# Kernel tuning notes

Hardware: AMD Instinct MI355X
Metric: run time of the kernel (lower is better)

## Reference

```python
import jax, jax.numpy as jnp
import numpy as np

N_NODES = 100000
N_EDGES = 1600000
DIM = 128
N_BUNDLES = 8
BUNDLE_DIM = 4
HIDDEN = 256
TIME = 2


def setup_inputs() -> dict:
    key = jax.random.key(0)
    ks = jax.random.split(key, 8)
    x = jax.random.normal(ks[0], (N_NODES, DIM), dtype=jnp.float32)
    node_rep = jax.random.normal(ks[1], (N_NODES, N_BUNDLES, BUNDLE_DIM, BUNDLE_DIM), dtype=jnp.float32)
    # edge list; ensure every node has out-degree >= 1 so degree norm is finite
    src_extra = jax.random.randint(ks[2], (N_EDGES - N_NODES,), 0, N_NODES)
    src = jnp.concatenate([jnp.arange(N_NODES), src_extra]).astype(jnp.int64)
    dst = jax.random.randint(ks[3], (N_EDGES,), 0, N_NODES).astype(jnp.int64)
    w1 = jax.random.normal(ks[4], (HIDDEN, DIM), dtype=jnp.float32) * (1.0 / np.sqrt(DIM))
    b1 = jnp.zeros((HIDDEN,), dtype=jnp.float32)
    w2 = jax.random.normal(ks[5], (DIM, HIDDEN), dtype=jnp.float32) * (1.0 / np.sqrt(HIDDEN))
    b2 = jnp.zeros((DIM,), dtype=jnp.float32)
    return {"x": x, "node_rep": node_rep, "src": src, "dst": dst,
            "w1": w1, "b1": b1, "w2": w2, "b2": b2}


def reference(x, node_rep, src, dst, w1, b1, w2, b2):
    n = x.shape[0]
    # out-degrees (number of edges with node as source)
    deg = jax.ops.segment_sum(jnp.ones_like(src, dtype=x.dtype), src, num_segments=n)
    # u_mul_v: per-edge product of src and dst degrees -> symmetric norm coefs
    norm_coefs = jax.lax.rsqrt(deg[src] * deg[dst])  # [E]
    # per-bundle rotation: einsum('abcd,abde->abce', node_rep, vf)
    vf = x.reshape(n, N_BUNDLES, BUNDLE_DIM, -1)
    vf = jnp.einsum('nbcd,nbde->nbce', node_rep, vf)
    h = vf.reshape(n, DIM)
    # u_mul_e_sum repeated `time` times: out[dst] += h[src] * coef
    for _ in range(TIME):
        h = jax.ops.segment_sum(h[src] * norm_coefs[:, None], dst, num_segments=n)
    # inverse rotation with transposed node_rep
    vf = h.reshape(n, N_BUNDLES, BUNDLE_DIM, -1)
    vf = jnp.einsum('nbdc,nbde->nbce', node_rep, vf)
    h = vf.reshape(n, DIM)
    # feed-forward (dropout=0, exact GELU as in torch nn.GELU default)
    h = jax.nn.gelu(h @ w1.T + b1, approximate=False)
    return h @ w2.T + b2
```

## Files before the change

kernel.cpp:

```cpp
#include <hip/hip_runtime.h>
#include <hip/hip_bf16.h>
#include <math.h>

#define DIM 128
#define HID 256

typedef short s8x __attribute__((ext_vector_type(8)));
typedef float f4x __attribute__((ext_vector_type(4)));

__device__ __forceinline__ unsigned short f2bf(float f) {
    unsigned int u = __float_as_uint(f);
    u += 0x7FFF + ((u >> 16) & 1);
    return (unsigned short)(u >> 16);
}
__device__ __forceinline__ float bf2f(unsigned short b) {
    return __uint_as_float(((unsigned int)b) << 16);
}
__device__ __forceinline__ float bflo(unsigned int p) {
    return __uint_as_float(p << 16);
}
__device__ __forceinline__ float bfhi(unsigned int p) {
    return __uint_as_float(p & 0xffff0000u);
}


__global__ __launch_bounds__(256) void hist_rot_kernel(
        const int* __restrict__ src, const int* __restrict__ dst,
        int* __restrict__ TD, int* __restrict__ TS, int nE, int nbuck, int chunk,
        int NBE,
        const float* __restrict__ x, const float* __restrict__ R,
        unsigned short* __restrict__ h0,
        const float* __restrict__ w1, const float* __restrict__ w2,
        unsigned short* __restrict__ w1b, unsigned short* __restrict__ w2b,
        int n, int nbRot) {
    __shared__ int hd[1024], hs[1024];
    const int tid = threadIdx.x, blk = blockIdx.x;

    if (blk >= NBE) {
        const int rb = blk - NBE;
        if (rb >= nbRot) {
            int t = (rb - nbRot) * 256 + tid;
            for (int i = t; i < 32768; i += 4096) {
                w1b[i] = f2bf(w1[i]);
                w2b[i] = f2bf(w2[i]);
            }
            return;
        }
        int u = rb * 256 + tid;
        if (u >= n * 8) return;
        int nd = u >> 3, b = u & 7;
        const float* xp = &x[(size_t)nd * DIM + b * 16];
        const float* Rp = &R[(size_t)nd * DIM + b * 16];
        float xv[16], rv[16];
#pragma unroll
        for (int d = 0; d < 4; ++d) {
            *(float4*)&xv[d * 4] = *(const float4*)&xp[d * 4];
            *(float4*)&rv[d * 4] = *(const float4*)&Rp[d * 4];
        }
        unsigned short ob[16];
#pragma unroll
        for (int c = 0; c < 4; ++c)
#pragma unroll
            for (int e = 0; e < 4; ++e) {
                float acc = 0.f;
#pragma unroll
                for (int d = 0; d < 4; ++d) acc += rv[c * 4 + d] * xv[d * 4 + e];
                ob[c * 4 + e] = f2bf(acc);
            }
        unsigned short* op = &h0[(size_t)nd * DIM + b * 16];
        *(s8x*)&op[0] = *(s8x*)&ob[0];
        *(s8x*)&op[8] = *(s8x*)&ob[8];
        return;
    }

    for (int b = tid; b < nbuck; b += 256) { hd[b] = 0; hs[b] = 0; }
    __syncthreads();
    int beg = blk * chunk, end = min(beg + chunk, nE);
    for (int i = beg + tid; i < end; i += 256) {
        atomicAdd(&hd[dst[i] >> 7], 1);
        atomicAdd(&hs[src[i] >> 7], 1);
    }
    __syncthreads();
    for (int b = tid; b < nbuck; b += 256) {
        TD[b * NBE + blk] = hd[b];
        TS[b * NBE + blk] = hs[b];
    }
}

__global__ void scan_blocks(const int* in, int* out, int* bsums, int n) {
    __shared__ int part[256];
    const int tid = threadIdx.x;
    const int base = blockIdx.x * 1024 + tid * 4;
    int v[4];
    int sum = 0;
#pragma unroll
    for (int k = 0; k < 4; ++k) {
        v[k] = (base + k < n) ? in[base + k] : 0;
        sum += v[k];
    }
    part[tid] = sum;
    __syncthreads();
    for (int off = 1; off < 256; off <<= 1) {
        int t = (tid >= off) ? part[tid - off] : 0;
        __syncthreads();
        part[tid] += t;
        __syncthreads();
    }
    int excl = part[tid] - sum;
    if (tid == 255) bsums[blockIdx.x] = part[255];
#pragma unroll
    for (int k = 0; k < 4; ++k) {
        if (base + k < n) out[base + k] = excl;
        excl += v[k];
    }
}

__global__ void scan_sums(int* bsums, int nb) {
    __shared__ int part[256];
    const int tid = threadIdx.x;
    const int base = tid * 8;
    int v[8];
    int sum = 0;
#pragma unroll
    for (int k = 0; k < 8; ++k) {
        v[k] = (base + k < nb) ? bsums[base + k] : 0;
        sum += v[k];
    }
    part[tid] = sum;
    __syncthreads();
    for (int off = 1; off < 256; off <<= 1) {
        int t = (tid >= off) ? part[tid - off] : 0;
        __syncthreads();
        part[tid] += t;
        __syncthreads();
    }
    int excl = part[tid] - sum;
#pragma unroll
    for (int k = 0; k < 8; ++k) {
        if (base + k < nb) bsums[base + k] = excl;
        excl += v[k];
    }
}

__global__ void scan_add(int* T, const int* __restrict__ bsums, int n2, int half, int E) {
    int i = blockIdx.x * blockDim.x + threadIdx.x;
    if (i < n2) {
        int v = T[i] + bsums[i >> 10];
        T[i] = (i >= half) ? v - E : v;
    }
}

__global__ __launch_bounds__(256) void scatter_edges(
        const int* __restrict__ src, const int* __restrict__ dst,
        const int* __restrict__ TD, const int* __restrict__ TS,
        unsigned int* __restrict__ pairs, unsigned char* __restrict__ sbyte,
        int nE, int nbuck, int chunk, int NBE) {
    __shared__ int cd[1024], cs[1024];
    const int tid = threadIdx.x, blk = blockIdx.x;
    for (int b = tid; b < nbuck; b += 256) {
        cd[b] = TD[b * NBE + blk];
        cs[b] = TS[b * NBE + blk];
    }
    __syncthreads();
    int beg = blk * chunk, end = min(beg + chunk, nE);
    for (int i = beg + tid; i < end; i += 256) {
        int s = src[i], d = dst[i];
        int pd = atomicAdd(&cd[d >> 7], 1);
        pairs[pd] = ((unsigned)s << 7) | (unsigned)(d & 127);
        int ps = atomicAdd(&cs[s >> 7], 1);
        sbyte[ps] = (unsigned char)(s & 127);
    }
}

__global__ __launch_bounds__(256) void finalize_src(
        const unsigned char* __restrict__ sbyte, const int* __restrict__ TS,
        float* __restrict__ rdeg, int nE, int nbuck, int nN, int NBE) {
    __shared__ int hist[128];
    const int tid = threadIdx.x, b = blockIdx.x;
    if (tid < 128) hist[tid] = 0;
    __syncthreads();
    int beg = TS[b * NBE];
    int end = (b + 1 < nbuck) ? TS[(b + 1) * NBE] : nE;
    for (int i = beg + tid; i < end; i += 256)
        atomicAdd(&hist[sbyte[i]], 1);
    __syncthreads();
    if (tid < 128) {
        int idx = (b << 7) + tid;
        if (idx < nN) rdeg[idx] = rsqrtf((float)hist[tid]);
    }
}

template<bool PACK>
__global__ __launch_bounds__(256) void finalize_dst(
        const unsigned int* __restrict__ pairs, const int* __restrict__ TD,
        const float* __restrict__ rdeg,
        int* __restrict__ rowstart, uint2* __restrict__ ecsr,
        int* __restrict__ esrcA, int nE, int nbuck, int nN, int NBE) {
    __shared__ int hist[128], sbuf[128], cur[128];
    const int tid = threadIdx.x, b = blockIdx.x;
    int beg = TD[b * NBE];
    int end = (b + 1 < nbuck) ? TD[(b + 1) * NBE] : nE;
    if (tid < 128) hist[tid] = 0;
    __syncthreads();
    for (int i = beg + tid; i < end; i += 256)
        atomicAdd(&hist[(int)(pairs[i] & 127u)], 1);
    __syncthreads();
    int v = (tid < 128) ? hist[tid] : 0;
    if (tid < 128) sbuf[tid] = v;
    __syncthreads();
    for (int off = 1; off < 128; off <<= 1) {
        int t = (tid < 128 && tid >= off) ? sbuf[tid - off] : 0;
        __syncthreads();
        if (tid < 128) sbuf[tid] += t;
        __syncthreads();
    }
    if (tid < 128) {
        int excl = sbuf[tid] - v;
        cur[tid] = excl;
        int idx = (b << 7) + tid;
        if (idx <= nN) rowstart[idx] = beg + excl;
    }
    __syncthreads();
    for (int i = beg + tid; i < end; i += 256) {
        unsigned int p = pairs[i];
        int l = (int)(p & 127u);
        int s = (int)(p >> 7);
        int pos = atomicAdd(&cur[l], 1);
        if (PACK) {
            float coef = rdeg[s] * rdeg[(b << 7) + l];
            ecsr[beg + pos] = make_uint2((unsigned)s, __float_as_uint(coef));
        } else {
            esrcA[beg + pos] = s;
        }
    }
}

template<bool PACK, bool ROT>
__global__ __launch_bounds__(256) void gather_kernel(
        const unsigned short* __restrict__ hsrc,
        const uint2* __restrict__ ecsr, const int* __restrict__ esrcA,
        const float* __restrict__ rdeg, const int* __restrict__ rowstart,
        const float* __restrict__ R,
        unsigned short* __restrict__ hdst, int n) {
    const int node = blockIdx.x * 16 + (threadIdx.x >> 4);
    const int lane = threadIdx.x & 15;
    if (node >= n) return;
    const int beg = rowstart[node];
    const int end = rowstart[node + 1];
    float rd = 0.f;
    if (!PACK) rd = rdeg[node];

    float4 r0, r1;
    if (ROT) {
        r0 = *(const float4*)&R[(size_t)node * DIM + lane * 8];
        r1 = *(const float4*)&R[(size_t)node * DIM + lane * 8 + 4];
    }

    float a0 = 0.f, a1 = 0.f, a2 = 0.f, a3 = 0.f;
    float a4 = 0.f, a5 = 0.f, a6 = 0.f, a7 = 0.f;
    int i = beg;
    for (; i + 4 <= end; i += 4) {
        int s0, s1, s2, s3;
        float c0, c1, c2, c3;
        if (PACK) {
            uint2 e0 = ecsr[i], e1 = ecsr[i + 1], e2 = ecsr[i + 2], e3 = ecsr[i + 3];
            s0 = (int)e0.x; c0 = __uint_as_float(e0.y);
            s1 = (int)e1.x; c1 = __uint_as_float(e1.y);
            s2 = (int)e2.x; c2 = __uint_as_float(e2.y);
            s3 = (int)e3.x; c3 = __uint_as_float(e3.y);
        } else {
            s0 = esrcA[i]; s1 = esrcA[i + 1]; s2 = esrcA[i + 2]; s3 = esrcA[i + 3];
            c0 = rdeg[s0] * rd; c1 = rdeg[s1] * rd;
            c2 = rdeg[s2] * rd; c3 = rdeg[s3] * rd;
        }
        uint4 p0 = *(const uint4*)&hsrc[(size_t)s0 * DIM + lane * 8];
        uint4 p1 = *(const uint4*)&hsrc[(size_t)s1 * DIM + lane * 8];
        uint4 p2 = *(const uint4*)&hsrc[(size_t)s2 * DIM + lane * 8];
        uint4 p3 = *(const uint4*)&hsrc[(size_t)s3 * DIM + lane * 8];
        a0 += bflo(p0.x) * c0 + bflo(p1.x) * c1 + bflo(p2.x) * c2 + bflo(p3.x) * c3;
        a1 += bfhi(p0.x) * c0 + bfhi(p1.x) * c1 + bfhi(p2.x) * c2 + bfhi(p3.x) * c3;
        a2 += bflo(p0.y) * c0 + bflo(p1.y) * c1 + bflo(p2.y) * c2 + bflo(p3.y) * c3;
        a3 += bfhi(p0.y) * c0 + bfhi(p1.y) * c1 + bfhi(p2.y) * c2 + bfhi(p3.y) * c3;
        a4 += bflo(p0.z) * c0 + bflo(p1.z) * c1 + bflo(p2.z) * c2 + bflo(p3.z) * c3;
        a5 += bfhi(p0.z) * c0 + bfhi(p1.z) * c1 + bfhi(p2.z) * c2 + bfhi(p3.z) * c3;
        a6 += bflo(p0.w) * c0 + bflo(p1.w) * c1 + bflo(p2.w) * c2 + bflo(p3.w) * c3;
        a7 += bfhi(p0.w) * c0 + bfhi(p1.w) * c1 + bfhi(p2.w) * c2 + bfhi(p3.w) * c3;
    }
    for (; i < end; ++i) {
        int s0;
        float c0;
        if (PACK) {
            uint2 e0 = ecsr[i];
            s0 = (int)e0.x; c0 = __uint_as_float(e0.y);
        } else {
            s0 = esrcA[i];
            c0 = rdeg[s0] * rd;
        }
        uint4 p0 = *(const uint4*)&hsrc[(size_t)s0 * DIM + lane * 8];
        a0 += bflo(p0.x) * c0;
        a1 += bfhi(p0.x) * c0;
        a2 += bflo(p0.y) * c0;
        a3 += bfhi(p0.y) * c0;
        a4 += bflo(p0.z) * c0;
        a5 += bfhi(p0.z) * c0;
        a6 += bflo(p0.w) * c0;
        a7 += bfhi(p0.w) * c0;
    }

    unsigned short ob[8];
    if (ROT) {
        const int half = lane & 1;
        float av[8] = {a0, a1, a2, a3, a4, a5, a6, a7};
        float rown[8] = {r0.x, r0.y, r0.z, r0.w, r1.x, r1.y, r1.z, r1.w};
        float hb[16], rv[16];
#pragma unroll
        for (int j = 0; j < 8; ++j) {
            float ho = __shfl_xor(av[j], 1);
            float ro = __shfl_xor(rown[j], 1);
            hb[j]     = half ? ho      : av[j];
            hb[8 + j] = half ? av[j]   : ho;
            rv[j]     = half ? ro      : rown[j];
            rv[8 + j] = half ? rown[j] : ro;
        }
        float rr[2][4];
#pragma unroll
        for (int cc = 0; cc < 2; ++cc)
#pragma unroll
            for (int d = 0; d < 4; ++d)
                rr[cc][d] = half ? rv[d * 4 + 2 + cc] : rv[d * 4 + cc];
#pragma unroll
        for (int cc = 0; cc < 2; ++cc)
#pragma unroll
            for (int e = 0; e < 4; ++e) {
                float acc = 0.f;
#pragma unroll
                for (int d = 0; d < 4; ++d) acc += rr[cc][d] * hb[d * 4 + e];
                ob[cc * 4 + e] = f2bf(acc);
            }
    } else {
        ob[0] = f2bf(a0); ob[1] = f2bf(a1); ob[2] = f2bf(a2); ob[3] = f2bf(a3);
        ob[4] = f2bf(a4); ob[5] = f2bf(a5); ob[6] = f2bf(a6); ob[7] = f2bf(a7);
    }
    uint4 o;
    o.x = (unsigned)ob[0] | ((unsigned)ob[1] << 16);
    o.y = (unsigned)ob[2] | ((unsigned)ob[3] << 16);
    o.z = (unsigned)ob[4] | ((unsigned)ob[5] << 16);
    o.w = (unsigned)ob[6] | ((unsigned)ob[7] << 16);
    *(uint4*)&hdst[(size_t)node * DIM + lane * 8] = o;
}

#define ABST 136
#define HBST 264
__global__ __launch_bounds__(256, 4) void ffn_kernel(
        const unsigned short* __restrict__ h,
        const unsigned short* __restrict__ w1b,
        const float* __restrict__ b1,
        const unsigned short* __restrict__ w2b,
        const float* __restrict__ b2,
        float* __restrict__ out, int n) {
    __shared__ unsigned short smem[64 * HBST];
    unsigned short* abuf = smem;
    unsigned short* hbuf = smem;
    const int tid  = threadIdx.x;
    const int node0 = blockIdx.x * 64;
    const int wave = tid >> 6;
    const int lane = tid & 63;
    const int lr = lane & 15;
    const int lq = lane >> 4;

    for (int u = tid; u < 512; u += 256) {
        int nd = u >> 3, b = u & 7;
        int gn = node0 + nd;
        s8x v0 = {0,0,0,0,0,0,0,0}, v1 = {0,0,0,0,0,0,0,0};
        if (gn < n) {
            const unsigned short* hp = &h[(size_t)gn * DIM + b * 16];
            v0 = *(const s8x*)&hp[0];
            v1 = *(const s8x*)&hp[8];
        }
        *(s8x*)&abuf[nd * ABST + b * 16] = v0;
        *(s8x*)&abuf[nd * ABST + b * 16 + 8] = v1;
    }
    __syncthreads();

    f4x acc1[4][4];
#pragma unroll
    for (int mt = 0; mt < 4; ++mt)
#pragma unroll
        for (int nt = 0; nt < 4; ++nt) acc1[mt][nt] = (f4x){0.f, 0.f, 0.f, 0.f};

    const int nw = wave * 64;
    for (int ks = 0; ks < 4; ++ks) {
        const int k0 = ks * 32 + lq * 8;
        s8x af[4], bfv[4];
#pragma unroll
        for (int mt = 0; mt < 4; ++mt)
            af[mt] = *(const s8x*)&abuf[(mt * 16 + lr) * ABST + k0];
#pragma unroll
        for (int nt = 0; nt < 4; ++nt)
            bfv[nt] = *(const s8x*)&w1b[(size_t)(nw + nt * 16 + lr) * 128 + k0];
#pragma unroll
        for (int mt = 0; mt < 4; ++mt)
#pragma unroll
            for (int nt = 0; nt < 4; ++nt)
                acc1[mt][nt] = __builtin_amdgcn_mfma_f32_16x16x32_bf16(
                    af[mt], bfv[nt], acc1[mt][nt], 0, 0, 0);
    }
    __syncthreads();

#pragma unroll
    for (int nt = 0; nt < 4; ++nt) {
        int nn = nw + nt * 16 + lr;
        float bias = b1[nn];
#pragma unroll
        for (int mt = 0; mt < 4; ++mt) {
#pragma unroll
            for (int r = 0; r < 4; ++r) {
                float v = acc1[mt][nt][r] + bias;
                v = 0.5f * v * (1.f + erff(v * 0.70710678118654752f));
                hbuf[(mt * 16 + lq * 4 + r) * HBST + nn] = f2bf(v);
            }
        }
    }
    __syncthreads();

    f4x acc2[4][2];
#pragma unroll
    for (int mt = 0; mt < 4; ++mt)
#pragma unroll
        for (int nt = 0; nt < 2; ++nt) acc2[mt][nt] = (f4x){0.f, 0.f, 0.f, 0.f};

    const int nw2 = wave * 32;
    for (int ks = 0; ks < 8; ++ks) {
        const int k0 = ks * 32 + lq * 8;
        s8x af[4], bf2v[2];
#pragma unroll
        for (int mt = 0; mt < 4; ++mt)
            af[mt] = *(const s8x*)&hbuf[(mt * 16 + lr) * HBST + k0];
#pragma unroll
        for (int nt = 0; nt < 2; ++nt)
            bf2v[nt] = *(const s8x*)&w2b[(size_t)(nw2 + nt * 16 + lr) * 256 + k0];
#pragma unroll
        for (int mt = 0; mt < 4; ++mt)
#pragma unroll
            for (int nt = 0; nt < 2; ++nt)
                acc2[mt][nt] = __builtin_amdgcn_mfma_f32_16x16x32_bf16(
                    af[mt], bf2v[nt], acc2[mt][nt], 0, 0, 0);
    }
#pragma unroll
    for (int nt = 0; nt < 2; ++nt) {
        int n2 = nw2 + nt * 16 + lr;
        float bias = b2[n2];
#pragma unroll
        for (int mt = 0; mt < 4; ++mt) {
#pragma unroll
            for (int r = 0; r < 4; ++r) {
                int gn = node0 + mt * 16 + lq * 4 + r;
                if (gn < n) out[(size_t)gn * DIM + n2] = acc2[mt][nt][r] + bias;
            }
        }
    }
}

extern "C" void kernel_launch(void* const* d_in, const int* in_sizes, int n_in,
                              void* d_out, int out_size, void* d_ws, size_t ws_size,
                              hipStream_t stream) {
    const float* x   = (const float*)d_in[0];
    const float* R   = (const float*)d_in[1];
    const int*   src = (const int*)d_in[2];
    const int*   dst = (const int*)d_in[3];
    const float* w1  = (const float*)d_in[4];
    const float* b1  = (const float*)d_in[5];
    const float* w2  = (const float*)d_in[6];
    const float* b2  = (const float*)d_in[7];
    float* out = (float*)d_out;

    const int N = in_sizes[0] / DIM;
    const int E = in_sizes[2];

    const int nbuck = (N + 127) >> 7;
    const int NBE = 256;
    const int chunk = (E + NBE - 1) / NBE;
    const int nScan = nbuck * NBE;
    const int nScan2 = 2 * nScan;
    const int nbScan2 = (nScan2 + 1023) / 1024;

    unsigned short* hA = (unsigned short*)d_ws;
    unsigned short* hM = hA + (size_t)N * DIM;
    unsigned int*  pairs = (unsigned int*)hM;
    unsigned char* sbyte = (unsigned char*)(pairs + E);
    char* edge_base = (char*)(hM + (size_t)N * DIM);

    const size_t tail_bytes = (size_t)N * 4 + (size_t)(N + 1) * 4 +
                              (size_t)nScan * 8 + 2048 * 4 + (size_t)2 * 32768 * 2;
    const size_t fixed_bytes = (size_t)N * DIM * 4;
    const bool use_pack = (fixed_bytes + (size_t)E * 8 + tail_bytes) <= ws_size;
    const size_t edge_bytes = use_pack ? (size_t)E * 8 : (size_t)E * 4;

    uint2* ecsr  = (uint2*)edge_base;
    int*   esrcA = (int*)edge_base;
    char* q = edge_base + edge_bytes;
    float* rdeg     = (float*)q;
    int*   rowstart = (int*)(rdeg + N);
    int*   TD       = rowstart + (N + 1);
    int*   TS       = TD + nScan;
    int*   bsums    = TS + nScan;
    unsigned short* w1b = (unsigned short*)(bsums + 2048);
    unsigned short* w2b = w1b + 32768;

    const int BLK = 256;

    const int nbRot = ((size_t)N * 8 + BLK - 1) / BLK;
    hist_rot_kernel<<<NBE + nbRot + 16, BLK, 0, stream>>>(
        src, dst, TD, TS, E, nbuck, chunk, NBE,
        x, R, hA, w1, w2, w1b, w2b, N, nbRot);

    scan_blocks<<<nbScan2, BLK, 0, stream>>>(TD, TD, bsums, nScan2);
    scan_sums<<<1, BLK, 0, stream>>>(bsums, nbScan2);
    scan_add<<<(nScan2 + BLK - 1) / BLK, BLK, 0, stream>>>(TD, bsums, nScan2, nScan, E);
    scatter_edges<<<NBE, BLK, 0, stream>>>(src, dst, TD, TS, pairs, sbyte, E, nbuck, chunk, NBE);
    finalize_src<<<nbuck, BLK, 0, stream>>>(sbyte, TS, rdeg, E, nbuck, N, NBE);
    if (use_pack)
        finalize_dst<true><<<nbuck, BLK, 0, stream>>>(pairs, TD, rdeg, rowstart,
                                                      ecsr, esrcA, E, nbuck, N, NBE);
    else
        finalize_dst<false><<<nbuck, BLK, 0, stream>>>(pairs, TD, rdeg, rowstart,
                                                       ecsr, esrcA, E, nbuck, N, NBE);

    const int nbG = (N + 15) / 16;
    if (use_pack) {
        gather_kernel<true , false><<<nbG, BLK, 0, stream>>>(hA, ecsr, esrcA, rdeg,
                                                             rowstart, R, hM, N);
        gather_kernel<true , true ><<<nbG, BLK, 0, stream>>>(hM, ecsr, esrcA, rdeg,
                                                             rowstart, R, hA, N);
    } else {
        gather_kernel<false, false><<<nbG, BLK, 0, stream>>>(hA, ecsr, esrcA, rdeg,
                                                             rowstart, R, hM, N);
        gather_kernel<false, true ><<<nbG, BLK, 0, stream>>>(hM, ecsr, esrcA, rdeg,
                                                             rowstart, R, hA, N);
    }

    ffn_kernel<<<(N + 63) / 64, BLK, 0, stream>>>(hA, w1b, b1, w2b, b2, out, N);
}
```

Baseline: 418.7 us.

## Unroll edge histogram/scatter and SpMM gather; load FFN A-tiles directly from global

```diff
diff --git a/kernel.cpp b/kernel.cpp
--- a/kernel.cpp
+++ b/kernel.cpp
@@ -76,7 +76,16 @@
     for (int b = tid; b < nbuck; b += 256) { hd[b] = 0; hs[b] = 0; }
     __syncthreads();
     int beg = blk * chunk, end = min(beg + chunk, nE);
-    for (int i = beg + tid; i < end; i += 256) {
+    int i = beg + tid;
+    for (; i + 256 < end; i += 512) {
+        int d0 = dst[i], d1 = dst[i + 256];
+        int s0 = src[i], s1 = src[i + 256];
+        atomicAdd(&hd[d0 >> 7], 1);
+        atomicAdd(&hd[d1 >> 7], 1);
+        atomicAdd(&hs[s0 >> 7], 1);
+        atomicAdd(&hs[s1 >> 7], 1);
+    }
+    if (i < end) {
         atomicAdd(&hd[dst[i] >> 7], 1);
         atomicAdd(&hs[src[i] >> 7], 1);
     }
@@ -163,7 +172,20 @@
     }
     __syncthreads();
     int beg = blk * chunk, end = min(beg + chunk, nE);
-    for (int i = beg + tid; i < end; i += 256) {
+    int i = beg + tid;
+    for (; i + 256 < end; i += 512) {
+        int s0 = src[i], d0 = dst[i];
+        int s1 = src[i + 256], d1 = dst[i + 256];
+        int pd0 = atomicAdd(&cd[d0 >> 7], 1);
+        pairs[pd0] = ((unsigned)s0 << 7) | (unsigned)(d0 & 127);
+        int pd1 = atomicAdd(&cd[d1 >> 7], 1);
+        pairs[pd1] = ((unsigned)s1 << 7) | (unsigned)(d1 & 127);
+        int ps0 = atomicAdd(&cs[s0 >> 7], 1);
+        sbyte[ps0] = (unsigned char)(s0 & 127);
+        int ps1 = atomicAdd(&cs[s1 >> 7], 1);
+        sbyte[ps1] = (unsigned char)(s1 & 127);
+    }
+    if (i < end) {
         int s = src[i], d = dst[i];
         int pd = atomicAdd(&cd[d >> 7], 1);
         pairs[pd] = ((unsigned)s << 7) | (unsigned)(d & 127);
@@ -259,6 +281,53 @@
     float a0 = 0.f, a1 = 0.f, a2 = 0.f, a3 = 0.f;
     float a4 = 0.f, a5 = 0.f, a6 = 0.f, a7 = 0.f;
     int i = beg;
+    for (; i + 8 <= end; i += 8) {
+        int s0, s1, s2, s3, s4, s5, s6, s7;
+        float c0, c1, c2, c3, c4, c5, c6, c7;
+        if (PACK) {
+            uint2 e0 = ecsr[i],     e1 = ecsr[i + 1], e2 = ecsr[i + 2], e3 = ecsr[i + 3];
+            uint2 e4 = ecsr[i + 4], e5 = ecsr[i + 5], e6 = ecsr[i + 6], e7 = ecsr[i + 7];
+            s0 = (int)e0.x; c0 = __uint_as_float(e0.y);
+            s1 = (int)e1.x; c1 = __uint_as_float(e1.y);
+            s2 = (int)e2.x; c2 = __uint_as_float(e2.y);
+            s3 = (int)e3.x; c3 = __uint_as_float(e3.y);
+            s4 = (int)e4.x; c4 = __uint_as_float(e4.y);
+            s5 = (int)e5.x; c5 = __uint_as_float(e5.y);
+            s6 = (int)e6.x; c6 = __uint_as_float(e6.y);
+            s7 = (int)e7.x; c7 = __uint_as_float(e7.y);
+        } else {
+            s0 = esrcA[i];     s1 = esrcA[i + 1]; s2 = esrcA[i + 2]; s3 = esrcA[i + 3];
+            s4 = esrcA[i + 4]; s5 = esrcA[i + 5]; s6 = esrcA[i + 6]; s7 = esrcA[i + 7];
+            c0 = rdeg[s0] * rd; c1 = rdeg[s1] * rd;
+            c2 = rdeg[s2] * rd; c3 = rdeg[s3] * rd;
+            c4 = rdeg[s4] * rd; c5 = rdeg[s5] * rd;
+            c6 = rdeg[s6] * rd; c7 = rdeg[s7] * rd;
+        }
+        uint4 p0 = *(const uint4*)&hsrc[(size_t)s0 * DIM + lane * 8];
+        uint4 p1 = *(const uint4*)&hsrc[(size_t)s1 * DIM + lane * 8];
+        uint4 p2 = *(const uint4*)&hsrc[(size_t)s2 * DIM + lane * 8];
+        uint4 p3 = *(const uint4*)&hsrc[(size_t)s3 * DIM + lane * 8];
+        uint4 p4 = *(const uint4*)&hsrc[(size_t)s4 * DIM + lane * 8];
+        uint4 p5 = *(const uint4*)&hsrc[(size_t)s5 * DIM + lane * 8];
+        uint4 p6 = *(const uint4*)&hsrc[(size_t)s6 * DIM + lane * 8];
+        uint4 p7 = *(const uint4*)&hsrc[(size_t)s7 * DIM + lane * 8];
+        a0 += bflo(p0.x) * c0 + bflo(p1.x) * c1 + bflo(p2.x) * c2 + bflo(p3.x) * c3
+            + bflo(p4.x) * c4 + bflo(p5.x) * c5 + bflo(p6.x) * c6 + bflo(p7.x) * c7;
+        a1 += bfhi(p0.x) * c0 + bfhi(p1.x) * c1 + bfhi(p2.x) * c2 + bfhi(p3.x) * c3
+            + bfhi(p4.x) * c4 + bfhi(p5.x) * c5 + bfhi(p6.x) * c6 + bfhi(p7.x) * c7;
+        a2 += bflo(p0.y) * c0 + bflo(p1.y) * c1 + bflo(p2.y) * c2 + bflo(p3.y) * c3
+            + bflo(p4.y) * c4 + bflo(p5.y) * c5 + bflo(p6.y) * c6 + bflo(p7.y) * c7;
+        a3 += bfhi(p0.y) * c0 + bfhi(p1.y) * c1 + bfhi(p2.y) * c2 + bfhi(p3.y) * c3
+            + bfhi(p4.y) * c4 + bfhi(p5.y) * c5 + bfhi(p6.y) * c6 + bfhi(p7.y) * c7;
+        a4 += bflo(p0.z) * c0 + bflo(p1.z) * c1 + bflo(p2.z) * c2 + bflo(p3.z) * c3
+            + bflo(p4.z) * c4 + bflo(p5.z) * c5 + bflo(p6.z) * c6 + bflo(p7.z) * c7;
+        a5 += bfhi(p0.z) * c0 + bfhi(p1.z) * c1 + bfhi(p2.z) * c2 + bfhi(p3.z) * c3
+            + bfhi(p4.z) * c4 + bfhi(p5.z) * c5 + bfhi(p6.z) * c6 + bfhi(p7.z) * c7;
+        a6 += bflo(p0.w) * c0 + bflo(p1.w) * c1 + bflo(p2.w) * c2 + bflo(p3.w) * c3
+            + bflo(p4.w) * c4 + bflo(p5.w) * c5 + bflo(p6.w) * c6 + bflo(p7.w) * c7;
+        a7 += bfhi(p0.w) * c0 + bfhi(p1.w) * c1 + bfhi(p2.w) * c2 + bfhi(p3.w) * c3
+            + bfhi(p4.w) * c4 + bfhi(p5.w) * c5 + bfhi(p6.w) * c6 + bfhi(p7.w) * c7;
+    }
     for (; i + 4 <= end; i += 4) {
         int s0, s1, s2, s3;
         float c0, c1, c2, c3;
@@ -349,7 +418,6 @@
     *(uint4*)&hdst[(size_t)node * DIM + lane * 8] = o;
 }
 
-#define ABST 136
 #define HBST 264
 __global__ __launch_bounds__(256, 4) void ffn_kernel(
         const unsigned short* __restrict__ h,
@@ -358,9 +426,7 @@
         const unsigned short* __restrict__ w2b,
         const float* __restrict__ b2,
         float* __restrict__ out, int n) {
-    __shared__ unsigned short smem[64 * HBST];
-    unsigned short* abuf = smem;
-    unsigned short* hbuf = smem;
+    __shared__ unsigned short hbuf[64 * HBST];
     const int tid  = threadIdx.x;
     const int node0 = blockIdx.x * 64;
     const int wave = tid >> 6;
@@ -368,19 +434,7 @@
     const int lr = lane & 15;
     const int lq = lane >> 4;
 
-    for (int u = tid; u < 512; u += 256) {
-        int nd = u >> 3, b = u & 7;
-        int gn = node0 + nd;
-        s8x v0 = {0,0,0,0,0,0,0,0}, v1 = {0,0,0,0,0,0,0,0};
-        if (gn < n) {
-            const unsigned short* hp = &h[(size_t)gn * DIM + b * 16];
-            v0 = *(const s8x*)&hp[0];
-            v1 = *(const s8x*)&hp[8];
-        }
-        *(s8x*)&abuf[nd * ABST + b * 16] = v0;
-        *(s8x*)&abuf[nd * ABST + b * 16 + 8] = v1;
-    }
-    __syncthreads();
+    const unsigned short* hbase = &h[(size_t)node0 * DIM];
 
     f4x acc1[4][4];
 #pragma unroll
@@ -389,12 +443,13 @@
         for (int nt = 0; nt < 4; ++nt) acc1[mt][nt] = (f4x){0.f, 0.f, 0.f, 0.f};
 
     const int nw = wave * 64;
+#pragma unroll
     for (int ks = 0; ks < 4; ++ks) {
         const int k0 = ks * 32 + lq * 8;
         s8x af[4], bfv[4];
 #pragma unroll
         for (int mt = 0; mt < 4; ++mt)
-            af[mt] = *(const s8x*)&abuf[(mt * 16 + lr) * ABST + k0];
+            af[mt] = *(const s8x*)&hbase[(size_t)(mt * 16 + lr) * DIM + k0];
 #pragma unroll
         for (int nt = 0; nt < 4; ++nt)
             bfv[nt] = *(const s8x*)&w1b[(size_t)(nw + nt * 16 + lr) * 128 + k0];
@@ -405,7 +460,6 @@
                 acc1[mt][nt] = __builtin_amdgcn_mfma_f32_16x16x32_bf16(
                     af[mt], bfv[nt], acc1[mt][nt], 0, 0, 0);
     }
-    __syncthreads();
 
 #pragma unroll
     for (int nt = 0; nt < 4; ++nt) {
@@ -430,6 +484,7 @@
         for (int nt = 0; nt < 2; ++nt) acc2[mt][nt] = (f4x){0.f, 0.f, 0.f, 0.f};
 
     const int nw2 = wave * 32;
+#pragma unroll
     for (int ks = 0; ks < 8; ++ks) {
         const int k0 = ks * 32 + lq * 8;
         s8x af[4], bf2v[2];
```

After: 416.8 us. No clear change (-0.5%).

## Unroll edge histogram/scatter loops, use nontemporal stores, load FFN inputs directly

Applied to the files above, without the earlier changes.

```diff
diff --git a/kernel.cpp b/kernel.cpp
--- a/kernel.cpp
+++ b/kernel.cpp
@@ -7,6 +7,7 @@
 
 typedef short s8x __attribute__((ext_vector_type(8)));
 typedef float f4x __attribute__((ext_vector_type(4)));
+typedef unsigned int u4x __attribute__((ext_vector_type(4)));
 
 __device__ __forceinline__ unsigned short f2bf(float f) {
     unsigned int u = __float_as_uint(f);
@@ -76,7 +77,16 @@
     for (int b = tid; b < nbuck; b += 256) { hd[b] = 0; hs[b] = 0; }
     __syncthreads();
     int beg = blk * chunk, end = min(beg + chunk, nE);
-    for (int i = beg + tid; i < end; i += 256) {
+    int i = beg + tid;
+    for (; i + 256 < end; i += 512) {
+        int d0 = dst[i], d1 = dst[i + 256];
+        int s0 = src[i], s1 = src[i + 256];
+        atomicAdd(&hd[d0 >> 7], 1);
+        atomicAdd(&hd[d1 >> 7], 1);
+        atomicAdd(&hs[s0 >> 7], 1);
+        atomicAdd(&hs[s1 >> 7], 1);
+    }
+    if (i < end) {
         atomicAdd(&hd[dst[i] >> 7], 1);
         atomicAdd(&hs[src[i] >> 7], 1);
     }
@@ -163,7 +173,20 @@
     }
     __syncthreads();
     int beg = blk * chunk, end = min(beg + chunk, nE);
-    for (int i = beg + tid; i < end; i += 256) {
+    int i = beg + tid;
+    for (; i + 256 < end; i += 512) {
+        int s0 = src[i], d0 = dst[i];
+        int s1 = src[i + 256], d1 = dst[i + 256];
+        int pd0 = atomicAdd(&cd[d0 >> 7], 1);
+        pairs[pd0] = ((unsigned)s0 << 7) | (unsigned)(d0 & 127);
+        int pd1 = atomicAdd(&cd[d1 >> 7], 1);
+        pairs[pd1] = ((unsigned)s1 << 7) | (unsigned)(d1 & 127);
+        int ps0 = atomicAdd(&cs[s0 >> 7], 1);
+        sbyte[ps0] = (unsigned char)(s0 & 127);
+        int ps1 = atomicAdd(&cs[s1 >> 7], 1);
+        sbyte[ps1] = (unsigned char)(s1 & 127);
+    }
+    if (i < end) {
         int s = src[i], d = dst[i];
         int pd = atomicAdd(&cd[d >> 7], 1);
         pairs[pd] = ((unsigned)s << 7) | (unsigned)(d & 127);
@@ -341,15 +364,14 @@
         ob[0] = f2bf(a0); ob[1] = f2bf(a1); ob[2] = f2bf(a2); ob[3] = f2bf(a3);
         ob[4] = f2bf(a4); ob[5] = f2bf(a5); ob[6] = f2bf(a6); ob[7] = f2bf(a7);
     }
-    uint4 o;
+    u4x o;
     o.x = (unsigned)ob[0] | ((unsigned)ob[1] << 16);
     o.y = (unsigned)ob[2] | ((unsigned)ob[3] << 16);
     o.z = (unsigned)ob[4] | ((unsigned)ob[5] << 16);
     o.w = (unsigned)ob[6] | ((unsigned)ob[7] << 16);
-    *(uint4*)&hdst[(size_t)node * DIM + lane * 8] = o;
-}
-
-#define ABST 136
+    __builtin_nontemporal_store(o, (u4x*)&hdst[(size_t)node * DIM + lane * 8]);
+}
+
 #define HBST 264
 __global__ __launch_bounds__(256, 4) void ffn_kernel(
         const unsigned short* __restrict__ h,
@@ -358,9 +380,7 @@
         const unsigned short* __restrict__ w2b,
         const float* __restrict__ b2,
         float* __restrict__ out, int n) {
-    __shared__ unsigned short smem[64 * HBST];
-    unsigned short* abuf = smem;
-    unsigned short* hbuf = smem;
+    __shared__ unsigned short hbuf[64 * HBST];
     const int tid  = threadIdx.x;
     const int node0 = blockIdx.x * 64;
     const int wave = tid >> 6;
@@ -368,19 +388,7 @@
     const int lr = lane & 15;
     const int lq = lane >> 4;
 
-    for (int u = tid; u < 512; u += 256) {
-        int nd = u >> 3, b = u & 7;
-        int gn = node0 + nd;
-        s8x v0 = {0,0,0,0,0,0,0,0}, v1 = {0,0,0,0,0,0,0,0};
-        if (gn < n) {
-            const unsigned short* hp = &h[(size_t)gn * DIM + b * 16];
-            v0 = *(const s8x*)&hp[0];
-            v1 = *(const s8x*)&hp[8];
-        }
-        *(s8x*)&abuf[nd * ABST + b * 16] = v0;
-        *(s8x*)&abuf[nd * ABST + b * 16 + 8] = v1;
-    }
-    __syncthreads();
+    const unsigned short* hbase = &h[(size_t)node0 * DIM];
 
     f4x acc1[4][4];
 #pragma unroll
@@ -389,12 +397,13 @@
         for (int nt = 0; nt < 4; ++nt) acc1[mt][nt] = (f4x){0.f, 0.f, 0.f, 0.f};
 
     const int nw = wave * 64;
+#pragma unroll
     for (int ks = 0; ks < 4; ++ks) {
         const int k0 = ks * 32 + lq * 8;
         s8x af[4], bfv[4];
 #pragma unroll
         for (int mt = 0; mt < 4; ++mt)
-            af[mt] = *(const s8x*)&abuf[(mt * 16 + lr) * ABST + k0];
+            af[mt] = *(const s8x*)&hbase[(size_t)(mt * 16 + lr) * DIM + k0];
 #pragma unroll
         for (int nt = 0; nt < 4; ++nt)
             bfv[nt] = *(const s8x*)&w1b[(size_t)(nw + nt * 16 + lr) * 128 + k0];
@@ -405,7 +414,6 @@
                 acc1[mt][nt] = __builtin_amdgcn_mfma_f32_16x16x32_bf16(
                     af[mt], bfv[nt], acc1[mt][nt], 0, 0, 0);
     }
-    __syncthreads();
 
 #pragma unroll
     for (int nt = 0; nt < 4; ++nt) {
@@ -430,6 +438,7 @@
         for (int nt = 0; nt < 2; ++nt) acc2[mt][nt] = (f4x){0.f, 0.f, 0.f, 0.f};
 
     const int nw2 = wave * 32;
+#pragma unroll
     for (int ks = 0; ks < 8; ++ks) {
         const int k0 = ks * 32 + lq * 8;
         s8x af[4], bf2v[2];
@@ -455,7 +464,9 @@
 #pragma unroll
             for (int r = 0; r < 4; ++r) {
                 int gn = node0 + mt * 16 + lq * 4 + r;
-                if (gn < n) out[(size_t)gn * DIM + n2] = acc2[mt][nt][r] + bias;
+                if (gn < n)
+                    __builtin_nontemporal_store(acc2[mt][nt][r] + bias,
+                                                &out[(size_t)gn * DIM + n2]);
             }
         }
     }
```

Measured after the change: 414.1 us. About the same (-1.1%).
